# Performance work log

Hardware: AMD Instinct MI355X
Metric: run time of the kernel (lower is better)

## Reference

```python
import jax
import jax.numpy as jnp
import numpy as np

N_WIRES = 4          # hardcoded by QLayer encoder (rx on wires 0..3)
H = N_WIRES          # hidden_dim must equal n_qubits for the gating elementwise math
T, B, D, TAGS = 512, 2048, 8, 16  # original unbinds dim 0, so dim0 = time, dim1 = batch


def apply_rx(state, theta, wire):
    """Apply RX(theta) on `wire`. state: (B,2,2,2,2) complex64, theta: (B,)."""
    st = jnp.moveaxis(state, 1 + wire, -1)
    a, b = st[..., 0], st[..., 1]
    th = theta[:, None, None, None] * 0.5
    c = jnp.cos(th)
    s = -1j * jnp.sin(th)
    st = jnp.stack([c * a + s * b, s * a + c * b], axis=-1)
    return jnp.moveaxis(st, -1, 1 + wire)


def apply_cnot(state, ctrl, tgt):
    st = jnp.moveaxis(state, (1 + ctrl, 1 + tgt), (-2, -1))  # (...,2,2)
    st = st.at[..., 1, :].set(st[..., 1, ::-1])
    return jnp.moveaxis(st, (-2, -1), (1 + ctrl, 1 + tgt))


def qlayer(angles, thetas):
    """QuantumQLSTM.QLayer: RX data encoding, trainable RX, CNOT ring, PauliZ expvals.
    angles: (B, 4) data angles; thetas: (4,) trainable RX angles -> (B, 4) expvals."""
    bsz = angles.shape[0]
    state = jnp.zeros((bsz, 16), jnp.complex64).at[:, 0].set(1.0)
    state = state.reshape(bsz, 2, 2, 2, 2)
    for w in range(N_WIRES):
        state = apply_rx(state, angles[:, w], w)
    for w in range(N_WIRES):
        state = apply_rx(state, jnp.broadcast_to(thetas[w], (bsz,)), w)
    for w in range(N_WIRES):  # cnot(w, w+1), last wraps to 0
        state = apply_cnot(state, w, (w + 1) % N_WIRES)
    probs = state.real ** 2 + state.imag ** 2  # (B,2,2,2,2)
    exps = []
    for w in range(N_WIRES):
        sign = jnp.array([1.0, -1.0], jnp.float32).reshape(
            [1] + [2 if i == w else 1 for i in range(N_WIRES)])
        exps.append(jnp.sum(probs * sign, axis=(1, 2, 3, 4)))
    return jnp.stack(exps, axis=-1)  # (B, 4)


def lstm_forward(x, w_gates, b_gates, rx_theta):
    # Faithful to torch: inputs.unbind(dim=0) -> scan over axis 0; batch = x.shape[1].
    bsz = x.shape[1]
    h0 = jnp.zeros((bsz, H), x.dtype)
    c0 = jnp.zeros((bsz, H), x.dtype)

    def step(carry, xt):
        hx, cx = carry
        comb = jnp.concatenate([xt, hx], axis=-1)                    # (B, D+H)
        pre = jnp.einsum('bd,gkd->gbk', comb, w_gates) + b_gates[:, None, :]  # (4,B,4)
        f = jax.nn.sigmoid(qlayer(pre[0], rx_theta[0]))
        i = jax.nn.sigmoid(qlayer(pre[1], rx_theta[1]))
        g = jnp.tanh(qlayer(pre[2], rx_theta[2]))
        o = jax.nn.sigmoid(qlayer(pre[3], rx_theta[3]))
        cx = f * cx + i * g
        hx = o * jnp.tanh(cx)
        return (hx, cx), hx

    _, outs = jax.lax.scan(jax.checkpoint(step), (h0, c0), x)
    return outs  # (T, B, H)


def setup_inputs() -> dict:
    key = jax.random.key(0)
    ks = jax.random.split(key, 6)
    x = jax.random.normal(ks[0], (T, B, D), jnp.float32)
    w_gates = jax.random.normal(ks[1], (4, N_WIRES, D + H), jnp.float32) * 0.3
    b_gates = jnp.zeros((4, N_WIRES), jnp.float32)
    rx_theta = jax.random.uniform(ks[2], (4, N_WIRES), jnp.float32, 0.0, 2.0 * np.pi)
    w_tag = jax.random.normal(ks[3], (TAGS, H), jnp.float32) * 0.3
    b_tag = jnp.zeros((TAGS,), jnp.float32)
    return {"x": x, "w_gates": w_gates, "b_gates": b_gates,
            "rx_theta": rx_theta, "w_tag": w_tag, "b_tag": b_tag}


def reference(x, w_gates, b_gates, rx_theta, w_tag, b_tag):
    # encode(): SamplerQNN has input_params=[], so it cannot transform features;
    # features pass through to the QLSTM (see notes).
    outs = lstm_forward(x, w_gates, b_gates, rx_theta)   # (T, B, H)
    logits = outs @ w_tag.T + b_tag                      # (T, B, TAGS)
    return jax.nn.log_softmax(logits, axis=-1)
```

## Files before the change

kernel.cpp:

```cpp
#include <hip/hip_runtime.h>

#define TT   512
#define BB   2048
#define NTAG 16
#define CH   8
#define NCH  (TT / CH)
#define BBN  (BB * NTAG)

typedef float v2f __attribute__((ext_vector_type(2)));

#define DPP_XOR1  0xB1
#define DPP_XOR2  0x4E
#define DPP_XOR3  0x1B
#define DPP_ROR4  0x124
#define DPP_ROR8  0x128
#define DPP_ROR12 0x12C
#define DPP_BC0   0x00
#define DPP_BC1   0x55
#define DPP_BC2   0xAA
#define DPP_BC3   0xFF

template<int CTRL>
__device__ __forceinline__ float dppf(float v) {
    int r = __builtin_amdgcn_update_dpp(0, __builtin_bit_cast(int, v),
                                        CTRL, 0xF, 0xF, true);
    return __builtin_bit_cast(float, r);
}

#define PINV(x) asm volatile("" : "+v"(x))

__global__ __launch_bounds__(256, 1) void qlstm_fused(
    const float* __restrict__ x,
    const float* __restrict__ w_gates,
    const float* __restrict__ b_gates,
    const float* __restrict__ rx_theta,
    const float* __restrict__ w_tag,
    const float* __restrict__ b_tag,
    float* __restrict__ out)
{
    __shared__ float  accL[2][2][CH][64];
    __shared__ float  hrng[2][2][CH][64];
    __shared__ float4 xstg[2][2][64];

    const int tid = threadIdx.x;
    const int wv  = tid >> 6;
    const int l   = tid & 63;
    const int e   = l >> 4;

    const float IV  = 0.15915494309189535f;
    const float L2E = 1.44269504088896f;
    const float LN2 = 0.69314718056f;

    if (wv < 2) {
        const int s = wv;
        const int w = (l >> 2) & 3;
        const int G = l & 3;

        const float* wrow = w_gates + (G * 4 + w) * 12;
        float wh0 = wrow[8 + ((w + 0) & 3)] * IV;
        float wh1 = wrow[8 + ((w + 1) & 3)] * IV;
        float wh2 = wrow[8 + ((w + 2) & 3)] * IV;
        float wh3 = wrow[8 + ((w + 3) & 3)] * IV;

        const bool gt = (G == 2);
        float ab = gt ? 0.0f : 0.5f;
        float d0 = gt ? 0.999904f  : 0.25f;
        float d1 = gt ? -0.331065f : -0.0208333333f;
        float d2 = gt ? 0.120472f  : 0.00208333333f;
        float d3 = gt ? -0.027717f : -2.10813e-4f;

        float u0 = 0.999160f,  u1 = -0.325289f, u2 = 0.112257f;
        float u3 = -0.028766f, u4 = 0.0043665f, u5 = -0.00028186f;

        const bool w0 = (w == 0), w1 = (w == 1), w3 = (w == 3);

        PINV(wh0); PINV(wh1); PINV(wh2); PINV(wh3);
        PINV(ab);  PINV(d0);  PINV(d1);  PINV(d2);  PINV(d3);
        PINV(u0);  PINV(u1);  PINV(u2);  PINV(u3);  PINV(u4);  PINV(u5);

        const int atl = (l & 48) | ((l & 3) << 2) | ((l >> 2) & 3);

        float h = 0.f, hg1 = 0.f, hg2 = 0.f, hg3 = 0.f, c = 0.f;

        __syncthreads();

        for (int cc = 0; cc < NCH; ++cc) {
            const int cur = cc & 1;

            const float* ap = &accL[s][cur][0][atl];
            float a0 = ap[0 * 64], a1 = ap[1 * 64];
            float a2 = ap[2 * 64], a3 = ap[3 * 64];
            float a4 = ap[4 * 64], a5 = ap[5 * 64];
            float a6 = ap[6 * 64], a7 = ap[7 * 64];
            asm volatile("" : "+v"(a0), "+v"(a1), "+v"(a2), "+v"(a3),
                             "+v"(a4), "+v"(a5), "+v"(a6), "+v"(a7));
            float a[CH] = { a0, a1, a2, a3, a4, a5, a6, a7 };

            float* hp = &hrng[s][cur][0][l];

            #pragma unroll
            for (int i = 0; i < CH; ++i) {
                const float sA  = fmaf(h, wh0, a[i]);
                const float td1 = fmaf(hg1, wh1, sA);
                const float td2 = hg2 * wh2;
                const float td3 = fmaf(hg3, wh3, td2);
                const float ang = td1 + td3;

                const float C = __builtin_amdgcn_cosf(ang);

                const float n1 = dppf<DPP_ROR12>(C);
                const float n2 = dppf<DPP_ROR8>(C);
                const float n3 = dppf<DPP_ROR4>(C);
                const float Bp = n2 * n3;
                const float pp = C * n1;
                const float F1  = w0 ? n1 : C;
                const float F1b = w3 ? pp : F1;
                const float F2  = w1 ? n3 : Bp;
                const float q   = F1b * F2;

                const float y  = q * q;
                const float y2 = y * y;
                const float tA = fmaf(y, d1, d0);
                const float tB = fmaf(y, d3, d2);
                const float P  = fmaf(y2, tB, tA);
                const float act = fmaf(q, P, ab);

                const float F_ = dppf<DPP_BC0>(act);
                const float A1 = dppf<DPP_BC1>(act);
                const float A2 = dppf<DPP_BC2>(act);
                const float O_ = dppf<DPP_BC3>(act);

                c = fmaf(F_, c, A1 * A2);

                const float cy  = c * c;
                const float cy2 = cy * cy;
                const float t1  = fmaf(cy, u1, u0);
                const float t2  = fmaf(cy, u3, u2);
                const float t3  = fmaf(cy, u5, u4);
                const float t4  = fmaf(cy2, t3, t2);
                const float Pc  = fmaf(cy2, t4, t1);
                const float voc = O_ * c;
                const float hr  = Pc * voc;

                hp[i * 64] = hr;

                h   = hr;
                hg1 = dppf<DPP_ROR12>(hr);
                hg2 = dppf<DPP_ROR8>(hr);
                hg3 = dppf<DPP_ROR4>(hr);
            }
            __syncthreads();
        }
    } else {
        const int s  = wv - 2;
        const int b0 = blockIdx.x * 8 + s * 4;
        const int g  = (l >> 2) & 3;
        const int k  = l & 3;

        const float* wrow = w_gates + (g * 4 + k) * 12;
        const v2f wp0 = { wrow[0] * IV, wrow[1] * IV };
        const v2f wp1 = { wrow[2] * IV, wrow[3] * IV };
        const v2f wp2 = { wrow[4] * IV, wrow[5] * IV };
        const v2f wp3 = { wrow[6] * IV, wrow[7] * IV };
        const v2f bp  = { (b_gates[g * 4 + k] + rx_theta[g * 4 + k]) * IV, 0.0f };

        const int tag = g * 4 + k;
        const float wt0 = w_tag[tag * 4 + (k ^ 0)] * L2E;
        const float wt1 = w_tag[tag * 4 + (k ^ 1)] * L2E;
        const float wt2 = w_tag[tag * 4 + (k ^ 2)] * L2E;
        const float wt3 = w_tag[tag * 4 + (k ^ 3)] * L2E;
        const float bt  = b_tag[tag] * L2E;

        const int hsl = e * 16 + k * 4;
        float* outp = out + (size_t)b0 * NTAG + l;

        const float* xlane = x + (size_t)(l >> 3) * (BB * 8)
                               + (size_t)b0 * 8 + (l & 7) * 4;
        const size_t CHOFF = (size_t)CH * BB * 8;

        float4 reg = *(const float4*)(xlane);
        xstg[s][0][l] = reg;
        reg = *(const float4*)(xlane + CHOFF);
        xstg[s][1][l] = reg;
        {
            float* ap = &accL[s][0][0][l];
            #pragma unroll
            for (int i = 0; i < CH; ++i) {
                const float4 xA = xstg[s][0][i * 8 + 2 * e];
                const float4 xB = xstg[s][0][i * 8 + 2 * e + 1];
                const v2f a01 = { xA.x, xA.y }, a23 = { xA.z, xA.w };
                const v2f a45 = { xB.x, xB.y }, a67 = { xB.z, xB.w };
                v2f acc = __builtin_elementwise_fma(a01, wp0, bp);
                acc = __builtin_elementwise_fma(a23, wp1, acc);
                acc = __builtin_elementwise_fma(a45, wp2, acc);
                acc = __builtin_elementwise_fma(a67, wp3, acc);
                ap[i * 64] = acc.x + acc.y;
            }
        }
        reg = *(const float4*)(xlane + 2 * CHOFF);
        __syncthreads();

        for (int cc = 0; cc < NCH; ++cc) {
            const int cur = cc & 1;

            if (cc + 2 < NCH) {
                xstg[s][cur][l] = reg;
                const int cn = (cc + 3 < NCH) ? cc + 3 : NCH - 1;
                reg = *(const float4*)(xlane + (size_t)cn * CHOFF);
            }

            if (cc + 1 < NCH) {
                float* ap = &accL[s][cur ^ 1][0][l];
                #pragma unroll
                for (int i = 0; i < CH; ++i) {
                    const float4 xA = xstg[s][cur ^ 1][i * 8 + 2 * e];
                    const float4 xB = xstg[s][cur ^ 1][i * 8 + 2 * e + 1];
                    const v2f a01 = { xA.x, xA.y }, a23 = { xA.z, xA.w };
                    const v2f a45 = { xB.x, xB.y }, a67 = { xB.z, xB.w };
                    v2f acc = __builtin_elementwise_fma(a01, wp0, bp);
                    acc = __builtin_elementwise_fma(a23, wp1, acc);
                    acc = __builtin_elementwise_fma(a45, wp2, acc);
                    acc = __builtin_elementwise_fma(a67, wp3, acc);
                    ap[i * 64] = acc.x + acc.y;
                }
            }

            if (cc > 0) {
                const float* hp = &hrng[s][cur ^ 1][0][hsl];
                #pragma unroll
                for (int i = 0; i < CH; ++i) {
                    const float hv = hp[i * 64];
                    const float q1 = dppf<DPP_XOR1>(hv);
                    const float q2 = dppf<DPP_XOR2>(hv);
                    const float q3 = dppf<DPP_XOR3>(hv);

                    const float lgq = fmaf(hv, wt0, fmaf(q1, wt1, fmaf(q2, wt2,
                                         fmaf(q3, wt3, bt))));
                    const float ex = __builtin_amdgcn_exp2f(lgq);
                    float sm = ex + dppf<DPP_XOR1>(ex);
                    sm = sm + dppf<DPP_XOR2>(sm);
                    sm = sm + dppf<DPP_ROR4>(sm);
                    sm = sm + dppf<DPP_ROR8>(sm);
                    const float l2s = __builtin_amdgcn_logf(sm);

                    *outp = (lgq - l2s) * LN2;
                    outp += BBN;
                }
            }
            __syncthreads();
        }

        {
            const float* hp = &hrng[s][1][0][hsl];
            #pragma unroll
            for (int i = 0; i < CH; ++i) {
                const float hv = hp[i * 64];
                const float q1 = dppf<DPP_XOR1>(hv);
                const float q2 = dppf<DPP_XOR2>(hv);
                const float q3 = dppf<DPP_XOR3>(hv);

                const float lgq = fmaf(hv, wt0, fmaf(q1, wt1, fmaf(q2, wt2,
                                     fmaf(q3, wt3, bt))));
                const float ex = __builtin_amdgcn_exp2f(lgq);
                float sm = ex + dppf<DPP_XOR1>(ex);
                sm = sm + dppf<DPP_XOR2>(sm);
                sm = sm + dppf<DPP_ROR4>(sm);
                sm = sm + dppf<DPP_ROR8>(sm);
                const float l2s = __builtin_amdgcn_logf(sm);

                *outp = (lgq - l2s) * LN2;
                outp += BBN;
            }
        }
    }
}

extern "C" void kernel_launch(void* const* d_in, const int* in_sizes, int n_in,
                              void* d_out, int out_size, void* d_ws, size_t ws_size,
                              hipStream_t stream) {
    const float* x        = (const float*)d_in[0];
    const float* w_gates  = (const float*)d_in[1];
    const float* b_gates  = (const float*)d_in[2];
    const float* rx_theta = (const float*)d_in[3];
    const float* w_tag    = (const float*)d_in[4];
    const float* b_tag    = (const float*)d_in[5];
    float* out = (float*)d_out;

    qlstm_fused<<<BB / 8, 256, 0, stream>>>(x, w_gates, b_gates, rx_theta,
                                            w_tag, b_tag, out);
}
```

Baseline: 137.6 us.

## Deepen accL ring to four stages and prefetch next chunk inside recurrence

```diff
diff --git a/kernel.cpp b/kernel.cpp
--- a/kernel.cpp
+++ b/kernel.cpp
@@ -38,7 +38,7 @@
     const float* __restrict__ b_tag,
     float* __restrict__ out)
 {
-    __shared__ float  accL[2][2][CH][64];
+    __shared__ float  accL[2][4][CH][64];
     __shared__ float  hrng[2][2][CH][64];
     __shared__ float4 xstg[2][2][64];
 
@@ -80,31 +80,32 @@
 
         const int atl = (l & 48) | ((l & 3) << 2) | ((l >> 2) & 3);
 
-        float h = 0.f, hg1 = 0.f, hg2 = 0.f, hg3 = 0.f, c = 0.f;
+        float h = 0.f, c = 0.f;
 
         __syncthreads();
 
+        float a[CH];
+        {
+            const float* ap0 = &accL[s][0][0][atl];
+            #pragma unroll
+            for (int i = 0; i < CH; ++i) a[i] = ap0[i * 64];
+        }
+
         for (int cc = 0; cc < NCH; ++cc) {
-            const int cur = cc & 1;
-
-            const float* ap = &accL[s][cur][0][atl];
-            float a0 = ap[0 * 64], a1 = ap[1 * 64];
-            float a2 = ap[2 * 64], a3 = ap[3 * 64];
-            float a4 = ap[4 * 64], a5 = ap[5 * 64];
-            float a6 = ap[6 * 64], a7 = ap[7 * 64];
-            asm volatile("" : "+v"(a0), "+v"(a1), "+v"(a2), "+v"(a3),
-                             "+v"(a4), "+v"(a5), "+v"(a6), "+v"(a7));
-            float a[CH] = { a0, a1, a2, a3, a4, a5, a6, a7 };
-
-            float* hp = &hrng[s][cur][0][l];
+            const float* np = &accL[s][(cc + 1) & 3][0][atl];
+            float n[CH];
+            #pragma unroll
+            for (int i = 0; i < CH; ++i) n[i] = np[i * 64];
+
+            float* hp = &hrng[s][cc & 1][0][l];
 
             #pragma unroll
             for (int i = 0; i < CH; ++i) {
-                const float sA  = fmaf(h, wh0, a[i]);
-                const float td1 = fmaf(hg1, wh1, sA);
-                const float td2 = hg2 * wh2;
-                const float td3 = fmaf(hg3, wh3, td2);
-                const float ang = td1 + td3;
+                const float s1 = fmaf(h, wh0, a[i]);
+                const float s2 = fmaf(dppf<DPP_ROR12>(h), wh1, s1);
+                const float mm = dppf<DPP_ROR8>(h) * wh2;
+                const float s3 = fmaf(dppf<DPP_ROR4>(h), wh3, mm);
+                const float ang = s2 + s3;
 
                 const float C = __builtin_amdgcn_cosf(ang);
 
@@ -125,30 +126,28 @@
                 const float P  = fmaf(y2, tB, tA);
                 const float act = fmaf(q, P, ab);
 
-                const float F_ = dppf<DPP_BC0>(act);
-                const float A1 = dppf<DPP_BC1>(act);
-                const float A2 = dppf<DPP_BC2>(act);
-                const float O_ = dppf<DPP_BC3>(act);
-
-                c = fmaf(F_, c, A1 * A2);
-
+                const float A2  = dppf<DPP_BC2>(act);
+                const float A12 = dppf<DPP_BC1>(act) * A2;
+                c = fmaf(dppf<DPP_BC0>(act), c, A12);
+
+                const float voc = dppf<DPP_BC3>(act) * c;
                 const float cy  = c * c;
                 const float cy2 = cy * cy;
                 const float t1  = fmaf(cy, u1, u0);
                 const float t2  = fmaf(cy, u3, u2);
                 const float t3  = fmaf(cy, u5, u4);
                 const float t4  = fmaf(cy2, t3, t2);
-                const float Pc  = fmaf(cy2, t4, t1);
-                const float voc = O_ * c;
-                const float hr  = Pc * voc;
+                const float m1v = voc * t1;
+                const float vc2 = voc * cy2;
+                const float hr  = fmaf(vc2, t4, m1v);
 
                 hp[i * 64] = hr;
-
-                h   = hr;
-                hg1 = dppf<DPP_ROR12>(hr);
-                hg2 = dppf<DPP_ROR8>(hr);
-                hg3 = dppf<DPP_ROR4>(hr);
-            }
+                h = hr;
+            }
+
+            #pragma unroll
+            for (int i = 0; i < CH; ++i) a[i] = n[i];
+
             __syncthreads();
         }
     } else {
@@ -178,16 +177,12 @@
                                + (size_t)b0 * 8 + (l & 7) * 4;
         const size_t CHOFF = (size_t)CH * BB * 8;
 
-        float4 reg = *(const float4*)(xlane);
-        xstg[s][0][l] = reg;
-        reg = *(const float4*)(xlane + CHOFF);
-        xstg[s][1][l] = reg;
-        {
-            float* ap = &accL[s][0][0][l];
+        auto compute_acc = [&](int xbuf, int ring) {
+            float* ap = &accL[s][ring][0][l];
             #pragma unroll
             for (int i = 0; i < CH; ++i) {
-                const float4 xA = xstg[s][0][i * 8 + 2 * e];
-                const float4 xB = xstg[s][0][i * 8 + 2 * e + 1];
+                const float4 xA = xstg[s][xbuf][i * 8 + 2 * e];
+                const float4 xB = xstg[s][xbuf][i * 8 + 2 * e + 1];
                 const v2f a01 = { xA.x, xA.y }, a23 = { xA.z, xA.w };
                 const v2f a45 = { xB.x, xB.y }, a67 = { xB.z, xB.w };
                 v2f acc = __builtin_elementwise_fma(a01, wp0, bp);
@@ -196,33 +191,28 @@
                 acc = __builtin_elementwise_fma(a67, wp3, acc);
                 ap[i * 64] = acc.x + acc.y;
             }
-        }
+        };
+
+        float4 reg = *(const float4*)(xlane);
+        xstg[s][0][l] = reg;
+        reg = *(const float4*)(xlane + CHOFF);
+        xstg[s][1][l] = reg;
+        compute_acc(0, 0);
+        compute_acc(1, 1);
         reg = *(const float4*)(xlane + 2 * CHOFF);
+        xstg[s][0][l] = reg;
+        reg = *(const float4*)(xlane + 3 * CHOFF);
         __syncthreads();
 
         for (int cc = 0; cc < NCH; ++cc) {
             const int cur = cc & 1;
 
-            if (cc + 2 < NCH) {
-                xstg[s][cur][l] = reg;
-                const int cn = (cc + 3 < NCH) ? cc + 3 : NCH - 1;
+            if (cc + 2 < NCH) compute_acc(cur, (cc + 2) & 3);
+
+            if (cc + 3 < NCH) {
+                xstg[s][cur ^ 1][l] = reg;
+                const int cn = (cc + 4 < NCH) ? cc + 4 : NCH - 1;
                 reg = *(const float4*)(xlane + (size_t)cn * CHOFF);
-            }
-
-            if (cc + 1 < NCH) {
-                float* ap = &accL[s][cur ^ 1][0][l];
-                #pragma unroll
-                for (int i = 0; i < CH; ++i) {
-                    const float4 xA = xstg[s][cur ^ 1][i * 8 + 2 * e];
-                    const float4 xB = xstg[s][cur ^ 1][i * 8 + 2 * e + 1];
-                    const v2f a01 = { xA.x, xA.y }, a23 = { xA.z, xA.w };
-                    const v2f a45 = { xB.x, xB.y }, a67 = { xB.z, xB.w };
-                    v2f acc = __builtin_elementwise_fma(a01, wp0, bp);
-                    acc = __builtin_elementwise_fma(a23, wp1, acc);
-                    acc = __builtin_elementwise_fma(a45, wp2, acc);
-                    acc = __builtin_elementwise_fma(a67, wp3, acc);
-                    ap[i * 64] = acc.x + acc.y;
-                }
             }
 
             if (cc > 0) {
```

Result: no change. 136.7 us (-0.7%).
